# Performance work log

Hardware: AMD Instinct MI355X
Metric: run time of the kernel (lower is better)

The kernel has to match this reference:

```python
import jax, jax.numpy as jnp
import numpy as np

N_NODES = 207
N_EDGES = 1722
N_SLOTS = 288
RESOLUTION = 1
BATCH = 1024


def setup_inputs() -> dict:
    key = jax.random.key(0)
    ks = jax.random.split(key, 8)
    inputs = jax.random.normal(ks[0], (BATCH, 2, 12, N_NODES), dtype=jnp.float32)
    weight_react = jax.random.normal(ks[1], (N_SLOTS, N_EDGES), dtype=jnp.float32) / 10.0
    weight_diff = jax.random.normal(ks[2], (N_SLOTS, N_EDGES), dtype=jnp.float32) / 1000.0
    bias_reaction = jax.random.normal(ks[3], (N_SLOTS, N_NODES), dtype=jnp.float32) / 10.0
    bias_diffusion = jax.random.normal(ks[4], (N_SLOTS, N_NODES), dtype=jnp.float32) / 10.0
    weight_self_loop = jax.random.normal(ks[5], (N_SLOTS, N_NODES), dtype=jnp.float32) / 10.0
    ind = jax.random.randint(ks[6], (BATCH,), 0, N_SLOTS, dtype=jnp.int32)
    edge_index = jax.random.randint(ks[7], (2, N_EDGES), 0, N_NODES, dtype=jnp.int32)
    return {
        'inputs': inputs,
        'weight_react': weight_react,
        'weight_diff': weight_diff,
        'bias_reaction': bias_reaction,
        'bias_diffusion': bias_diffusion,
        'weight_self_loop': weight_self_loop,
        'ind': ind,
        'edge_index': edge_index,
    }


def _build_adjacency(edge_index, vals):
    """Symmetric dense adjacency per batch element.

    edge_index: [2, E] int; vals: [B, E] float.
    Returns A [B, N, N] with A[b, i, j] += v and A[b, j, i] += v (duplicates summed,
    matching torch.sparse_coo_tensor coalescing).
    """
    src = jnp.concatenate([edge_index[0], edge_index[1]])  # [2E]
    dst = jnp.concatenate([edge_index[1], edge_index[0]])  # [2E]
    v = jnp.concatenate([vals, vals], axis=1)              # [B, 2E]
    B = vals.shape[0]
    A = jnp.zeros((B, N_NODES, N_NODES), dtype=vals.dtype)
    return A.at[:, src, dst].add(v)


def reference(inputs, weight_react, weight_diff, bias_reaction, bias_diffusion,
              weight_self_loop, ind, edge_index):
    B = inputs.shape[0]
    # [B, d1, d2, N] -> [B, d1*d2, N] -> [B, N, L]
    x = inputs.reshape(B, -1, N_NODES).transpose(0, 2, 1)
    ii = ind // RESOLUTION  # time-of-day slot per sample, [B]

    A_r = _build_adjacency(edge_index, weight_react[ii])  # [B, N, N]
    A_d = _build_adjacency(edge_index, weight_diff[ii])   # [B, N, N]
    diag = jnp.arange(N_NODES)
    # torch sums dim 1 of [N, N] (column sums) and adds/subtracts diag of it
    d_r = A_r.sum(axis=1)  # [B, N]
    d_d = A_d.sum(axis=1)  # [B, N]
    R = A_r.at[:, diag, diag].add(d_r)   # diag(d) + A
    D = (-A_d).at[:, diag, diag].add(d_d)  # diag(d) - A

    # nconv: out[b, w, l] = sum_v x[b, v, l] * A[b, w, v]
    reaction = jnp.einsum('bvl,bwv->bwl', x, R) + bias_reaction[ii][:, :, None]
    diffusion = jnp.einsum('bvl,bwv->bwl', x, D) + bias_diffusion[ii][:, :, None]
    self_loop = weight_self_loop[ii][:, :, None] * x
    return jnp.tanh(reaction) + diffusion + x + self_loop  # [B, N, L]
```

## Files before the change

kernel.cpp:

```cpp
#include <hip/hip_runtime.h>

#define N_NODES 207
#define N_EDGES 1722
#define N_SLOTS 288
#define L_DIM 24
#define NPK 12
#define TOT_ENT (2 * N_EDGES)

typedef float f32x2 __attribute__((ext_vector_type(2)));
typedef __fp16 h16x2 __attribute__((ext_vector_type(2)));

__device__ __forceinline__ unsigned pkrtz(float a, float b) {
    h16x2 h = __builtin_amdgcn_cvt_pkrtz(a, b);
    return __builtin_bit_cast(unsigned, h);
}
__device__ __forceinline__ f32x2 h2f(unsigned u) {
    h16x2 h = __builtin_bit_cast(h16x2, u);
    f32x2 r; r.x = (float)h.x; r.y = (float)h.y;
    return r;
}
__device__ __forceinline__ void fma_lo(unsigned& acc, unsigned wt, unsigned x) {
    asm("v_pk_fma_f16 %0, %1, %2, %0 op_sel:[0,0,0] op_sel_hi:[0,1,1]"
        : "+v"(acc) : "v"(wt), "v"(x));
}
__device__ __forceinline__ void fma_hi(unsigned& acc, unsigned wt, unsigned x) {
    asm("v_pk_fma_f16 %0, %1, %2, %0 op_sel:[1,0,0] op_sel_hi:[1,1,1]"
        : "+v"(acc) : "v"(wt), "v"(x));
}
__device__ __forceinline__ void addw(unsigned& sw, unsigned wt) {
    asm("v_pk_add_f16 %0, %1, %0" : "+v"(sw) : "v"(wt));
}
__device__ __forceinline__ float fast_tanhf(float x) {
    float e2 = __expf(2.0f * x);
    return 1.0f - 2.0f * __builtin_amdgcn_rcpf(e2 + 1.0f);
}

__global__ __launch_bounds__(256, 4) void rdgcn_fused_kernel(
    const float* __restrict__ x_in,
    const float* __restrict__ w_react,
    const float* __restrict__ w_diff,
    const float* __restrict__ b_react,
    const float* __restrict__ b_diff,
    const float* __restrict__ w_self,
    const int* __restrict__ ind,
    const int* __restrict__ edge_index,
    float* __restrict__ out)
{
    __shared__ unsigned x_sh[N_NODES * NPK];
    __shared__ unsigned wt_sh[N_EDGES];
    __shared__ unsigned ent_sh[TOT_ENT + 4];

    const int b    = blockIdx.x;
    const int tid  = threadIdx.x;
    const int lane = tid & 63;
    const int wid  = tid >> 6;
    const int s    = ind[b];

    int* cnt_s  = (int*)x_sh;
    int* cur_s  = cnt_s + 208;
    int* off_s  = cur_s + 208;
    int* perm_s = off_s + 209;
    int* dcur_s = perm_s + 208;
    int* wsum_s = dcur_s + 64;

    if (tid < 208) cnt_s[tid] = 0;
    if (tid < 64)  dcur_s[tid] = 0;
    __syncthreads();

    int ei[7], ej[7];
    int ne = 0;
    for (int e = tid; e < N_EDGES; e += 256) {
        int i = edge_index[e];
        int j = edge_index[N_EDGES + e];
        ei[ne] = i; ej[ne] = j; ++ne;
        atomicAdd(&cnt_s[i], 1);
        atomicAdd(&cnt_s[j], 1);
    }
    __syncthreads();

    const int deg = (tid < N_NODES) ? cnt_s[tid] : 0;
    int xs = deg;
    #pragma unroll
    for (int sft = 1; sft < 64; sft <<= 1) {
        int t = __shfl_up(xs, sft, 64);
        if (lane >= sft) xs += t;
    }
    if (lane == 63) wsum_s[wid] = xs;
    const int dcap = deg > 63 ? 63 : deg;
    if (tid < N_NODES) atomicAdd(&dcur_s[dcap], 1);
    __syncthreads();

    int base = 0;
    for (int i = 0; i < wid; ++i) base += wsum_s[i];
    const int excl = base + xs - deg;
    if (tid < N_NODES) { off_s[tid] = excl; cur_s[tid] = excl; }
    if (tid == 255)    off_s[N_NODES] = base + xs;

    if (tid < 64) {
        int h = dcur_s[63 - tid];
        int ys = h;
        #pragma unroll
        for (int sft = 1; sft < 64; sft <<= 1) {
            int t = __shfl_up(ys, sft, 64);
            if (lane >= sft) ys += t;
        }
        __syncthreads();
        dcur_s[63 - tid] = ys - h;
    } else {
        __syncthreads();
    }
    __syncthreads();

    if (tid < N_NODES) {
        int p = atomicAdd(&dcur_s[dcap], 1);
        perm_s[p] = tid;
    }
    for (int q = 0; q < ne; ++q) {
        const int i = ei[q], j = ej[q];
        const int e = tid + q * 256;
        int pi = atomicAdd(&cur_s[i], 1);
        ent_sh[pi] = (unsigned)j | ((unsigned)e << 16);
        int pj = atomicAdd(&cur_s[j], 1);
        ent_sh[pj] = (unsigned)i | ((unsigned)e << 16);
    }
    if (tid == 0) { ent_sh[TOT_ENT] = 0u; ent_sh[TOT_ENT + 1] = 0u; }
    __syncthreads();

    int w = 0, beg = 0, end = 0;
    if (tid < N_NODES) {
        w   = perm_s[tid];
        beg = off_s[w];
        end = off_s[w + 1];
    }
    __syncthreads();

    float br = 0.f, bd = 0.f, wsl = 0.f;
    if (tid < N_NODES) {
        br  = b_react[s * N_NODES + w];
        bd  = b_diff [s * N_NODES + w];
        wsl = w_self [s * N_NODES + w];
    }
    const float* xg = x_in + (size_t)b * (L_DIM * N_NODES);
    if (tid < N_NODES) {
        float r[L_DIM];
        #pragma unroll
        for (int l = 0; l < L_DIM; ++l) r[l] = xg[l * N_NODES + tid];
        unsigned p[NPK];
        #pragma unroll
        for (int i = 0; i < NPK; ++i) p[i] = pkrtz(r[2*i], r[2*i+1]);
        uint4* dst = reinterpret_cast<uint4*>(&x_sh[tid * NPK]);
        dst[0] = make_uint4(p[0], p[1], p[2],  p[3]);
        dst[1] = make_uint4(p[4], p[5], p[6],  p[7]);
        dst[2] = make_uint4(p[8], p[9], p[10], p[11]);
    }
    {
        const float* wrg = w_react + (size_t)s * N_EDGES;
        const float* wdg = w_diff  + (size_t)s * N_EDGES;
        for (int e = tid; e < N_EDGES; e += 256)
            wt_sh[e] = pkrtz(wrg[e], wdg[e]);
    }
    __syncthreads();

    if (tid >= N_NODES) return;

    unsigned accr[NPK] = {0,0,0,0,0,0,0,0,0,0,0,0};
    unsigned accd[NPK] = {0,0,0,0,0,0,0,0,0,0,0,0};
    unsigned sw = 0;

    unsigned en = ent_sh[beg];
    for (int k = beg; k < end; ++k) {
        const unsigned en_nx = ent_sh[k + 1];
        const int nbr = (int)(en & 0xffffu);
        const int e   = (int)(en >> 16);
        const unsigned wt = wt_sh[e];
        const uint4* xr = reinterpret_cast<const uint4*>(&x_sh[nbr * NPK]);
        const uint4 qa = xr[0], qb = xr[1], qc = xr[2];
        en = en_nx;
        addw(sw, wt);
        fma_lo(accr[0],  wt, qa.x);   fma_hi(accd[0],  wt, qa.x);
        fma_lo(accr[1],  wt, qa.y);   fma_hi(accd[1],  wt, qa.y);
        fma_lo(accr[2],  wt, qa.z);   fma_hi(accd[2],  wt, qa.z);
        fma_lo(accr[3],  wt, qa.w);   fma_hi(accd[3],  wt, qa.w);
        fma_lo(accr[4],  wt, qb.x);   fma_hi(accd[4],  wt, qb.x);
        fma_lo(accr[5],  wt, qb.y);   fma_hi(accd[5],  wt, qb.y);
        fma_lo(accr[6],  wt, qb.z);   fma_hi(accd[6],  wt, qb.z);
        fma_lo(accr[7],  wt, qb.w);   fma_hi(accd[7],  wt, qb.w);
        fma_lo(accr[8],  wt, qc.x);   fma_hi(accd[8],  wt, qc.x);
        fma_lo(accr[9],  wt, qc.y);   fma_hi(accd[9],  wt, qc.y);
        fma_lo(accr[10], wt, qc.z);   fma_hi(accd[10], wt, qc.z);
        fma_lo(accr[11], wt, qc.w);   fma_hi(accd[11], wt, qc.w);
    }

    const f32x2 sw2 = h2f(sw);
    const float swr = sw2.x, swd = sw2.y;

    const uint4* xw = reinterpret_cast<const uint4*>(&x_sh[w * NPK]);
    const uint4 r0 = xw[0], r1 = xw[1], r2 = xw[2];
    const unsigned own[NPK] = { r0.x, r0.y, r0.z, r0.w,
                                r1.x, r1.y, r1.z, r1.w,
                                r2.x, r2.y, r2.z, r2.w };

    float o[L_DIM];
    #pragma unroll
    for (int i = 0; i < NPK; ++i) {
        const f32x2 xv = h2f(own[i]);
        const f32x2 ar = h2f(accr[i]);
        const f32x2 ad = h2f(accd[i]);
        {
            float re = fmaf(swr, xv.x,  ar.x) + br;
            float di = fmaf(swd, xv.x, -ad.x) + bd;
            o[2*i]   = fast_tanhf(re) + di + fmaf(xv.x, wsl, xv.x);
        }
        {
            float re = fmaf(swr, xv.y,  ar.y) + br;
            float di = fmaf(swd, xv.y, -ad.y) + bd;
            o[2*i+1] = fast_tanhf(re) + di + fmaf(xv.y, wsl, xv.y);
        }
    }
    float* op = out + (size_t)b * (N_NODES * L_DIM) + (size_t)w * L_DIM;
    reinterpret_cast<float4*>(op)[0] = make_float4(o[0],  o[1],  o[2],  o[3]);
    reinterpret_cast<float4*>(op)[1] = make_float4(o[4],  o[5],  o[6],  o[7]);
    reinterpret_cast<float4*>(op)[2] = make_float4(o[8],  o[9],  o[10], o[11]);
    reinterpret_cast<float4*>(op)[3] = make_float4(o[12], o[13], o[14], o[15]);
    reinterpret_cast<float4*>(op)[4] = make_float4(o[16], o[17], o[18], o[19]);
    reinterpret_cast<float4*>(op)[5] = make_float4(o[20], o[21], o[22], o[23]);
}

extern "C" void kernel_launch(void* const* d_in, const int* in_sizes, int n_in,
                              void* d_out, int out_size, void* d_ws, size_t ws_size,
                              hipStream_t stream) {
    const float* x_in     = (const float*)d_in[0];
    const float* w_react  = (const float*)d_in[1];
    const float* w_diff   = (const float*)d_in[2];
    const float* b_react  = (const float*)d_in[3];
    const float* b_diff   = (const float*)d_in[4];
    const float* w_self   = (const float*)d_in[5];
    const int*   ind      = (const int*)d_in[6];
    const int*   edge_idx = (const int*)d_in[7];
    float* out = (float*)d_out;

    const int B = in_sizes[6];
    rdgcn_fused_kernel<<<B, 256, 0, stream>>>(x_in, w_react, w_diff,
                                              b_react, b_diff, w_self,
                                              ind, edge_idx, out);
}
```

Measured before the change: 27.04 us.

## Process two batch samples per block, sharing the edge CSR build

Each 512-thread block now handles two batch elements, so the graph's CSR structure and degree permutation are built once and shared by two samples. Each half keeps its own x and weight tiles in shared memory. The per-sample x loads are also issued at kernel start, overlapping the CSR construction. The cost is more shared memory and registers per block, and it assumes an even batch size.

```diff
diff --git a/kernel.cpp b/kernel.cpp
--- a/kernel.cpp
+++ b/kernel.cpp
@@ -6,6 +6,7 @@
 #define L_DIM 24
 #define NPK 12
 #define TOT_ENT (2 * N_EDGES)
+#define THREADS 512
 
 typedef float f32x2 __attribute__((ext_vector_type(2)));
 typedef __fp16 h16x2 __attribute__((ext_vector_type(2)));
@@ -35,7 +36,7 @@
     return 1.0f - 2.0f * __builtin_amdgcn_rcpf(e2 + 1.0f);
 }
 
-__global__ __launch_bounds__(256, 4) void rdgcn_fused_kernel(
+__global__ __launch_bounds__(THREADS, 4) void rdgcn_fused_kernel(
     const float* __restrict__ x_in,
     const float* __restrict__ w_react,
     const float* __restrict__ w_diff,
@@ -46,17 +47,26 @@
     const int* __restrict__ edge_index,
     float* __restrict__ out)
 {
-    __shared__ unsigned x_sh[N_NODES * NPK];
-    __shared__ unsigned wt_sh[N_EDGES];
+    __shared__ unsigned x_sh[2][N_NODES * NPK];
+    __shared__ unsigned wt_sh[2][N_EDGES];
     __shared__ unsigned ent_sh[TOT_ENT + 4];
 
-    const int b    = blockIdx.x;
     const int tid  = threadIdx.x;
+    const int h    = tid >> 8;
+    const int htid = tid & 255;
     const int lane = tid & 63;
     const int wid  = tid >> 6;
+    const int b    = blockIdx.x * 2 + h;
     const int s    = ind[b];
 
-    int* cnt_s  = (int*)x_sh;
+    float r[L_DIM];
+    if (htid < N_NODES) {
+        const float* xg = x_in + (size_t)b * (L_DIM * N_NODES);
+        #pragma unroll
+        for (int l = 0; l < L_DIM; ++l) r[l] = xg[l * N_NODES + htid];
+    }
+
+    int* cnt_s  = (int*)wt_sh;
     int* cur_s  = cnt_s + 208;
     int* off_s  = cur_s + 208;
     int* perm_s = off_s + 209;
@@ -67,9 +77,9 @@
     if (tid < 64)  dcur_s[tid] = 0;
     __syncthreads();
 
-    int ei[7], ej[7];
+    int ei[4], ej[4];
     int ne = 0;
-    for (int e = tid; e < N_EDGES; e += 256) {
+    for (int e = tid; e < N_EDGES; e += THREADS) {
         int i = edge_index[e];
         int j = edge_index[N_EDGES + e];
         ei[ne] = i; ej[ne] = j; ++ne;
@@ -78,34 +88,36 @@
     }
     __syncthreads();
 
-    const int deg = (tid < N_NODES) ? cnt_s[tid] : 0;
+    const int deg  = (tid < N_NODES) ? cnt_s[tid] : 0;
+    const int dcap = deg > 63 ? 63 : deg;
     int xs = deg;
-    #pragma unroll
-    for (int sft = 1; sft < 64; sft <<= 1) {
-        int t = __shfl_up(xs, sft, 64);
-        if (lane >= sft) xs += t;
-    }
-    if (lane == 63) wsum_s[wid] = xs;
-    const int dcap = deg > 63 ? 63 : deg;
+    if (tid < 256) {
+        #pragma unroll
+        for (int sft = 1; sft < 64; sft <<= 1) {
+            int t = __shfl_up(xs, sft, 64);
+            if (lane >= sft) xs += t;
+        }
+        if (lane == 63) wsum_s[wid] = xs;
+    }
     if (tid < N_NODES) atomicAdd(&dcur_s[dcap], 1);
     __syncthreads();
 
     int base = 0;
-    for (int i = 0; i < wid; ++i) base += wsum_s[i];
+    if (tid < 256) { for (int i = 0; i < wid; ++i) base += wsum_s[i]; }
     const int excl = base + xs - deg;
     if (tid < N_NODES) { off_s[tid] = excl; cur_s[tid] = excl; }
     if (tid == 255)    off_s[N_NODES] = base + xs;
 
     if (tid < 64) {
-        int h = dcur_s[63 - tid];
-        int ys = h;
+        int hg = dcur_s[63 - tid];
+        int ys = hg;
         #pragma unroll
         for (int sft = 1; sft < 64; sft <<= 1) {
             int t = __shfl_up(ys, sft, 64);
             if (lane >= sft) ys += t;
         }
         __syncthreads();
-        dcur_s[63 - tid] = ys - h;
+        dcur_s[63 - tid] = ys - hg;
     } else {
         __syncthreads();
     }
@@ -116,39 +128,32 @@
         perm_s[p] = tid;
     }
     for (int q = 0; q < ne; ++q) {
-        const int i = ei[q], j = ej[q];
-        const int e = tid + q * 256;
-        int pi = atomicAdd(&cur_s[i], 1);
-        ent_sh[pi] = (unsigned)j | ((unsigned)e << 16);
-        int pj = atomicAdd(&cur_s[j], 1);
-        ent_sh[pj] = (unsigned)i | ((unsigned)e << 16);
+        const int e = tid + q * THREADS;
+        int pi = atomicAdd(&cur_s[ei[q]], 1);
+        ent_sh[pi] = (unsigned)ej[q] | ((unsigned)e << 16);
+        int pj = atomicAdd(&cur_s[ej[q]], 1);
+        ent_sh[pj] = (unsigned)ei[q] | ((unsigned)e << 16);
     }
     if (tid == 0) { ent_sh[TOT_ENT] = 0u; ent_sh[TOT_ENT + 1] = 0u; }
     __syncthreads();
 
     int w = 0, beg = 0, end = 0;
-    if (tid < N_NODES) {
-        w   = perm_s[tid];
+    if (htid < N_NODES) {
+        w   = perm_s[htid];
         beg = off_s[w];
         end = off_s[w + 1];
     }
     __syncthreads();
 
     float br = 0.f, bd = 0.f, wsl = 0.f;
-    if (tid < N_NODES) {
+    if (htid < N_NODES) {
         br  = b_react[s * N_NODES + w];
         bd  = b_diff [s * N_NODES + w];
         wsl = w_self [s * N_NODES + w];
-    }
-    const float* xg = x_in + (size_t)b * (L_DIM * N_NODES);
-    if (tid < N_NODES) {
-        float r[L_DIM];
-        #pragma unroll
-        for (int l = 0; l < L_DIM; ++l) r[l] = xg[l * N_NODES + tid];
         unsigned p[NPK];
         #pragma unroll
         for (int i = 0; i < NPK; ++i) p[i] = pkrtz(r[2*i], r[2*i+1]);
-        uint4* dst = reinterpret_cast<uint4*>(&x_sh[tid * NPK]);
+        uint4* dst = reinterpret_cast<uint4*>(&x_sh[h][htid * NPK]);
         dst[0] = make_uint4(p[0], p[1], p[2],  p[3]);
         dst[1] = make_uint4(p[4], p[5], p[6],  p[7]);
         dst[2] = make_uint4(p[8], p[9], p[10], p[11]);
@@ -156,24 +161,26 @@
     {
         const float* wrg = w_react + (size_t)s * N_EDGES;
         const float* wdg = w_diff  + (size_t)s * N_EDGES;
-        for (int e = tid; e < N_EDGES; e += 256)
-            wt_sh[e] = pkrtz(wrg[e], wdg[e]);
-    }
-    __syncthreads();
-
-    if (tid >= N_NODES) return;
+        for (int e = htid; e < N_EDGES; e += 256)
+            wt_sh[h][e] = pkrtz(wrg[e], wdg[e]);
+    }
+    __syncthreads();
+
+    if (htid >= N_NODES) return;
 
     unsigned accr[NPK] = {0,0,0,0,0,0,0,0,0,0,0,0};
     unsigned accd[NPK] = {0,0,0,0,0,0,0,0,0,0,0,0};
     unsigned sw = 0;
 
+    const unsigned* wth = wt_sh[h];
+    const unsigned* xsh = x_sh[h];
     unsigned en = ent_sh[beg];
     for (int k = beg; k < end; ++k) {
         const unsigned en_nx = ent_sh[k + 1];
         const int nbr = (int)(en & 0xffffu);
         const int e   = (int)(en >> 16);
-        const unsigned wt = wt_sh[e];
-        const uint4* xr = reinterpret_cast<const uint4*>(&x_sh[nbr * NPK]);
+        const unsigned wt = wth[e];
+        const uint4* xr = reinterpret_cast<const uint4*>(&xsh[nbr * NPK]);
         const uint4 qa = xr[0], qb = xr[1], qc = xr[2];
         en = en_nx;
         addw(sw, wt);
@@ -194,7 +201,7 @@
     const f32x2 sw2 = h2f(sw);
     const float swr = sw2.x, swd = sw2.y;
 
-    const uint4* xw = reinterpret_cast<const uint4*>(&x_sh[w * NPK]);
+    const uint4* xw = reinterpret_cast<const uint4*>(&xsh[w * NPK]);
     const uint4 r0 = xw[0], r1 = xw[1], r2 = xw[2];
     const unsigned own[NPK] = { r0.x, r0.y, r0.z, r0.w,
                                 r1.x, r1.y, r1.z, r1.w,
@@ -240,7 +247,7 @@
     float* out = (float*)d_out;
 
     const int B = in_sizes[6];
-    rdgcn_fused_kernel<<<B, 256, 0, stream>>>(x_in, w_react, w_diff,
-                                              b_react, b_diff, w_self,
-                                              ind, edge_idx, out);
-}
+    rdgcn_fused_kernel<<<B / 2, THREADS, 0, stream>>>(x_in, w_react, w_diff,
+                                                      b_react, b_diff, w_self,
+                                                      ind, edge_idx, out);
+}
```

Measured after the change: 25.58 us. 5.4% less time.
